# Performance work log

Hardware: AMD Instinct MI355X
Metric: run time of the kernel (lower is better)

The kernel has to match this reference:

```python
import jax, jax.numpy as jnp
import numpy as np

HIDDEN = 768
HEADS = 12
HEAD_DIM = HIDDEN // HEADS
BETA = 0.5
BANDWIDTH = 1.0
D_INTRINSIC = 3
LN_EPS = 1e-12


def setup_inputs() -> dict:
    key = jax.random.key(0)
    ks = jax.random.split(key, 10)
    B, S, E = 2, 2048, HIDDEN
    sc = 1.0 / np.sqrt(E)
    return {
        "hidden_states": jax.random.normal(ks[0], (B, S, E), jnp.float32),
        "attention_mask": jnp.zeros((B, S), jnp.float32),
        "Wq": jax.random.normal(ks[1], (E, E), jnp.float32) * sc,
        "bq": jax.random.normal(ks[2], (E,), jnp.float32) * 0.02,
        "Wv": jax.random.normal(ks[3], (E, E), jnp.float32) * sc,
        "bv": jax.random.normal(ks[4], (E,), jnp.float32) * 0.02,
        "Wo": jax.random.normal(ks[5], (E, E), jnp.float32) * sc,
        "bo": jax.random.normal(ks[6], (E,), jnp.float32) * 0.02,
        "ln_g": jnp.ones((E,), jnp.float32),
        "ln_b": jnp.zeros((E,), jnp.float32),
    }


def _layernorm(x, g, b, eps=LN_EPS):
    mu = jnp.mean(x, axis=-1, keepdims=True)
    var = jnp.mean((x - mu) ** 2, axis=-1, keepdims=True)
    return (x - mu) * jax.lax.rsqrt(var + eps) * g + b


def reference(hidden_states, attention_mask, Wq, bq, Wv, bv, Wo, bo, ln_g, ln_b):
    B, S, E = hidden_states.shape
    H, D = HEADS, HEAD_DIM
    # projections (torch Linear: x @ W.T + b)
    q = (hidden_states @ Wq.T + bq).reshape(B, S, H, D).transpose(0, 2, 1, 3)  # [B,H,S,D]
    v = (hidden_states @ Wv.T + bv).reshape(B, S, H, D).transpose(0, 2, 1, 3)  # [B,H,S,D]
    # pairwise Euclidean distance (cdist) via norm expansion, safe sqrt
    qn = jnp.sum(q * q, axis=-1)  # [B,H,S]
    d2 = qn[:, :, :, None] + qn[:, :, None, :] - 2.0 * jnp.einsum("bhid,bhjd->bhij", q, q)
    dist = jnp.sqrt(jnp.maximum(d2, 1e-12))  # [B,H,S,S]
    # mask: positions with attention_mask < 0 get distance 2
    keep = (attention_mask >= 0)  # [B,S]
    pair_keep = keep[:, None, :, None] & keep[:, None, None, :]  # [B,1,S,S]
    dist = jnp.where(pair_keep, dist, 2.0)
    # power-law score + softmax
    attn_score = (1.0 + dist / (BANDWIDTH ** 0.5)) ** (-D_INTRINSIC - BETA)
    attn = jax.nn.softmax(attn_score, axis=-1)
    out = jnp.einsum("bhij,bhjd->bhid", attn, v)  # [B,H,S,D]
    out = out.transpose(0, 2, 1, 3).reshape(B, S, E)
    # ModelSelfOutput: dense + residual + LayerNorm (dropout=0, eval)
    out = out @ Wo.T + bo
    return _layernorm(out + hidden_states, ln_g, ln_b)
```

## Files before the change

kernel.cpp:

```cpp
#include <hip/hip_runtime.h>
#include <hip/hip_bf16.h>
#include <cstdint>
#include <cstddef>

#define S_LEN 2048
#define NH 12
#define HD 64
#define EDIM 768

typedef short bf16x8 __attribute__((ext_vector_type(8)));
typedef float f32x4  __attribute__((ext_vector_type(4)));
typedef float f32x2  __attribute__((ext_vector_type(2)));

__device__ __forceinline__ unsigned short f2bf(float f) {
    return __bfloat16_as_ushort(__float2bfloat16(f));
}
__device__ __forceinline__ float bf2f(unsigned short u) {
    union { unsigned int i; float f; } x;
    x.i = ((unsigned int)u) << 16;
    return x.f;
}
__device__ __forceinline__ float rsq_f32(float x) {
#if __has_builtin(__builtin_amdgcn_rsqf)
    return __builtin_amdgcn_rsqf(x);
#else
    return __builtin_amdgcn_rcpf(__builtin_amdgcn_sqrtf(x));
#endif
}

__global__ __launch_bounds__(256) void precast_kernel(
    const float* __restrict__ hs, const float* __restrict__ Wq,
    const float* __restrict__ Wv, const float* __restrict__ Wo,
    unsigned short* __restrict__ hsb, unsigned short* __restrict__ Wqvb,
    unsigned short* __restrict__ Wob)
{
    const int i4 = blockIdx.x * 256 + threadIdx.x;
    const float* src;
    unsigned short* dst;
    int rel;
    if (i4 < 786432)        { src = hs; dst = hsb;            rel = i4; }
    else if (i4 < 933888)   { src = Wq; dst = Wqvb;           rel = i4 - 786432; }
    else if (i4 < 1081344)  { src = Wv; dst = Wqvb + 589824;  rel = i4 - 933888; }
    else                    { src = Wo; dst = Wob;            rel = i4 - 1081344; }
    float4 v = ((const float4*)src)[rel];
    ushort4 o;
    o.x = f2bf(v.x); o.y = f2bf(v.y); o.z = f2bf(v.z); o.w = f2bf(v.w);
    ((ushort4*)dst)[rel] = o;
}

__global__ __launch_bounds__(256) void qv_gemm(
    const unsigned short* __restrict__ hsb, const unsigned short* __restrict__ Wqvb,
    const float* __restrict__ bq, const float* __restrict__ bv,
    unsigned short* __restrict__ Qb, unsigned short* __restrict__ Vt,
    float* __restrict__ qn)
{
    __shared__ __align__(16) unsigned short As[64][40];
    __shared__ __align__(16) unsigned short Bs[128][40];

    const int t  = threadIdx.x;
    const int m0 = blockIdx.y << 6;
    const int c0 = blockIdx.x << 7;
    const bool isQ = (c0 < EDIM);
    const float* bias = isQ ? bq : bv;
    const int cb = isQ ? c0 : (c0 - EDIM);

    const int w  = t >> 6;
    const int l  = t & 63;
    const int ll = l & 15;
    const int lq = l >> 4;
    const int wx = w & 1;
    const int wy = w >> 1;

    const int srowA = t & 63;
    const int skA   = (t >> 6) << 3;
    const int srowB = t & 127;
    const int skB   = (t >> 7) << 4;

    f32x4 acc[2][4];
#pragma unroll
    for (int m = 0; m < 2; m++)
#pragma unroll
        for (int n = 0; n < 4; n++) acc[m][n] = (f32x4){0.f, 0.f, 0.f, 0.f};

    for (int k0 = 0; k0 < EDIM; k0 += 32) {
        bf16x8 va  = *(const bf16x8*)(hsb  + (size_t)(m0 + srowA) * EDIM + k0 + skA);
        bf16x8 vb0 = *(const bf16x8*)(Wqvb + (size_t)(c0 + srowB) * EDIM + k0 + skB);
        bf16x8 vb1 = *(const bf16x8*)(Wqvb + (size_t)(c0 + srowB) * EDIM + k0 + skB + 8);
        __syncthreads();
        *(bf16x8*)&As[srowA][skA]     = va;
        *(bf16x8*)&Bs[srowB][skB]     = vb0;
        *(bf16x8*)&Bs[srowB][skB + 8] = vb1;
        __syncthreads();
        bf16x8 aF[2], bF[4];
#pragma unroll
        for (int m = 0; m < 2; m++)
            aF[m] = *(const bf16x8*)&As[(wy << 5) + (m << 4) + ll][lq << 3];
#pragma unroll
        for (int n = 0; n < 4; n++)
            bF[n] = *(const bf16x8*)&Bs[(wx << 6) + (n << 4) + ll][lq << 3];
#pragma unroll
        for (int m = 0; m < 2; m++)
#pragma unroll
            for (int n = 0; n < 4; n++)
                acc[m][n] = __builtin_amdgcn_mfma_f32_16x16x32_bf16(aF[m], bF[n], acc[m][n], 0, 0, 0);
    }

    const int hcol0 = cb + (wx << 6);
    const int h = hcol0 >> 6;
    const int rowbase = m0 + (wy << 5);
    const int b = rowbase >> 11;
    const int sbase = rowbase & 2047;

    if (isQ) {
#pragma unroll
        for (int m = 0; m < 2; m++) {
#pragma unroll
            for (int r = 0; r < 4; r++) {
                const int si = sbase + (m << 4) + (lq << 2) + r;
                unsigned short* qrow = Qb + ((size_t)(b * NH + h) * S_LEN + si) * HD;
                float qsq = 0.f;
#pragma unroll
                for (int n = 0; n < 4; n++) {
                    unsigned short u = f2bf(acc[m][n][r] + bias[hcol0 + (n << 4) + ll]);
                    qrow[(n << 4) + ll] = u;
                    float f = bf2f(u);
                    qsq += f * f;
                }
                qsq += __shfl_xor(qsq, 1);
                qsq += __shfl_xor(qsq, 2);
                qsq += __shfl_xor(qsq, 4);
                qsq += __shfl_xor(qsq, 8);
                if (ll == 0) qn[(b * NH + h) * S_LEN + si] = qsq;
            }
        }
    } else {
#pragma unroll
        for (int m = 0; m < 2; m++) {
            const int si = sbase + (m << 4) + (lq << 2);
#pragma unroll
            for (int n = 0; n < 4; n++) {
                ushort4 o;
                o.x = f2bf(acc[m][n][0] + bias[hcol0 + (n << 4) + ll]);
                o.y = f2bf(acc[m][n][1] + bias[hcol0 + (n << 4) + ll]);
                o.z = f2bf(acc[m][n][2] + bias[hcol0 + (n << 4) + ll]);
                o.w = f2bf(acc[m][n][3] + bias[hcol0 + (n << 4) + ll]);
                *(ushort4*)&Vt[((size_t)(b * NH + h) * HD + (n << 4) + ll) * S_LEN + si] = o;
            }
        }
    }
}

template<int CUR>
__device__ __forceinline__ void attn_tile32(
    int j0, int jn,
    const unsigned short* __restrict__ Qbase,
    const unsigned short* __restrict__ Vbase,
    const float* __restrict__ qnb, const float* __restrict__ mb,
    int ll, int lq,
    const bf16x8 (&aQ)[2][2],
    const f32x2 (&qni2)[2][2], const f32x2 (&keepi2)[2][2],
    const bf16x8& ones,
    f32x4 (&oacc)[2][4], f32x4 (&wacc)[2],
    bf16x8 (&nb0)[2], bf16x8 (&nb1)[2],
    bf16x8 (&vbuf)[2][4],
    float (&qnjv)[2][2], float (&kjm)[2][2],
    unsigned short (&Wt)[2][2][16][40])
{
    constexpr int PRV = CUR ^ 1;
    __builtin_amdgcn_wave_barrier();
#pragma unroll
    for (int m = 0; m < 4; m++)
        vbuf[CUR][m] = *(const bf16x8*)(Vbase + (size_t)((m << 4) + ll) * S_LEN + j0 + (lq << 3));
    f32x4 s[2][2];
#pragma unroll
    for (int s2 = 0; s2 < 2; s2++)
#pragma unroll
        for (int n = 0; n < 2; n++) {
            f32x4 c = (f32x4){0.f, 0.f, 0.f, 0.f};
            c = __builtin_amdgcn_mfma_f32_16x16x32_bf16(aQ[s2][0], nb0[n], c, 0, 0, 0);
            c = __builtin_amdgcn_mfma_f32_16x16x32_bf16(aQ[s2][1], nb1[n], c, 0, 0, 0);
            s[s2][n] = c;
        }
#pragma unroll
    for (int n = 0; n < 2; n++) {
        const unsigned short* bp = Qbase + (size_t)(jn + (n << 4) + ll) * HD + (lq << 3);
        nb0[n] = *(const bf16x8*)bp;
        nb1[n] = *(const bf16x8*)(bp + 32);
        int jc = jn + (n << 4) + ll;
        qnjv[PRV][n] = qnb[jc];
        kjm[PRV][n]  = (mb[jc] >= 0.f) ? 1.f : 0.f;
    }
#pragma unroll
    for (int s2 = 0; s2 < 2; s2++) {
        bf16x8 aP = *(const bf16x8*)&Wt[PRV][s2][ll][lq << 3];
#pragma unroll
        for (int m = 0; m < 4; m++)
            oacc[s2][m] = __builtin_amdgcn_mfma_f32_16x16x32_bf16(aP, vbuf[PRV][m], oacc[s2][m], 0, 0, 0);
        wacc[s2] = __builtin_amdgcn_mfma_f32_16x16x32_bf16(aP, ones, wacc[s2], 0, 0, 0);
    }
#pragma unroll
    for (int s2 = 0; s2 < 2; s2++)
#pragma unroll
        for (int n = 0; n < 2; n++) {
            const f32x2 qv = (f32x2)(qnjv[CUR][n]);
            const f32x2 kj = (f32x2)(kjm[CUR][n]);
#pragma unroll
            for (int pr = 0; pr < 2; pr++) {
                f32x2 sp = { s[s2][n][2*pr], s[s2][n][2*pr + 1] };
                f32x2 d2 = __builtin_elementwise_fma(sp, (f32x2)(-2.f), qni2[s2][pr] + qv);
                d2 = __builtin_elementwise_max(d2, (f32x2)(1e-12f));
                f32x2 dist = { __builtin_amdgcn_sqrtf(d2.x), __builtin_amdgcn_sqrtf(d2.y) };
                f32x2 km = keepi2[s2][pr] * kj;
                f32x2 x  = __builtin_elementwise_fma(km, dist + (f32x2)(-2.f), (f32x2)(3.f));
                f32x2 x2 = x * x;
                f32x2 x4 = x2 * x2;
                f32x2 x6 = x4 * x2;
                f32x2 x7 = x6 * x;
                f32x2 p  = { rsq_f32(x7.x), rsq_f32(x7.y) };
                f32x2 wv = __builtin_elementwise_fma(
                    __builtin_elementwise_fma(
                        __builtin_elementwise_fma(
                            __builtin_elementwise_fma((f32x2)(0.041666668f), p, (f32x2)(0.16666667f)),
                            p, (f32x2)(0.5f)),
                        p, (f32x2)(1.0f)),
                    p, (f32x2)(1.0f));
                union { float f; unsigned int u; } c0, c1;
                c0.f = wv.x; c1.f = wv.y;
                Wt[CUR][s2][(lq << 2) + 2*pr    ][(n << 4) + ll] = (unsigned short)((c0.u + 0x8000u) >> 16);
                Wt[CUR][s2][(lq << 2) + 2*pr + 1][(n << 4) + ll] = (unsigned short)((c1.u + 0x8000u) >> 16);
            }
        }
}

__global__ __launch_bounds__(256) void attn_kernel(
    const unsigned short* __restrict__ Qb, const unsigned short* __restrict__ Vt,
    const float* __restrict__ qn, const float* __restrict__ mask,
    unsigned short* __restrict__ AObf)
{
    __shared__ __align__(16) unsigned short Wt[4][2][2][16][40];

    const int t  = threadIdx.x;
    const int w  = t >> 6;
    const int l  = t & 63;
    const int ll = l & 15;
    const int lq = l >> 4;
    const int id = blockIdx.x;
    const int ib = id / 24;
    const int bh = id - ib * 24;
    const int b  = bh / NH;
    const int h  = bh - b * NH;
    const int iw = ib << 5;

    const unsigned short* Qbase = Qb + ((size_t)bh << 17);
    const unsigned short* Vbase = Vt + ((size_t)bh << 17);
    const float* qnb = qn + (bh << 11);
    const float* mb  = mask + (b << 11);

    unsigned short (&Wtw)[2][2][16][40] = Wt[w];

    const int tbase = w << 4;
    const int jb    = tbase << 5;

    bf16x8 aQ[2][2];
#pragma unroll
    for (int s2 = 0; s2 < 2; s2++) {
        const unsigned short* qp = Qbase + (size_t)(iw + (s2 << 4) + ll) * HD + (lq << 3);
        aQ[s2][0] = *(const bf16x8*)qp;
        aQ[s2][1] = *(const bf16x8*)(qp + 32);
    }

    f32x2 qni2[2][2], keepi2[2][2];
#pragma unroll
    for (int s2 = 0; s2 < 2; s2++)
#pragma unroll
        for (int pr = 0; pr < 2; pr++) {
            int r0 = iw + (s2 << 4) + (lq << 2) + 2*pr;
            qni2[s2][pr]   = (f32x2){ qnb[r0], qnb[r0 + 1] };
            keepi2[s2][pr] = (f32x2){ (mb[r0] >= 0.f) ? 1.f : 0.f,
                                      (mb[r0 + 1] >= 0.f) ? 1.f : 0.f };
        }

    bf16x8 ones;
#pragma unroll
    for (int i = 0; i < 8; i++) ones[i] = (short)0x3F80;

    f32x4 oacc[2][4];
#pragma unroll
    for (int s2 = 0; s2 < 2; s2++)
#pragma unroll
        for (int m = 0; m < 4; m++) oacc[s2][m] = (f32x4){0.f, 0.f, 0.f, 0.f};
    f32x4 wacc[2];
    wacc[0] = (f32x4){0.f, 0.f, 0.f, 0.f};
    wacc[1] = (f32x4){0.f, 0.f, 0.f, 0.f};

    bf16x8 nb0[2], nb1[2];
    float qnjv[2][2], kjm[2][2];
#pragma unroll
    for (int n = 0; n < 2; n++) {
        const unsigned short* bp = Qbase + (size_t)(jb + (n << 4) + ll) * HD + (lq << 3);
        nb0[n] = *(const bf16x8*)bp;
        nb1[n] = *(const bf16x8*)(bp + 32);
        int jc = jb + (n << 4) + ll;
        qnjv[0][n] = qnb[jc];
        kjm[0][n]  = (mb[jc] >= 0.f) ? 1.f : 0.f;
    }
    bf16x8 vbuf[2][4];

    {
#pragma unroll
        for (int m = 0; m < 4; m++)
            vbuf[0][m] = *(const bf16x8*)(Vbase + (size_t)((m << 4) + ll) * S_LEN + jb + (lq << 3));
        f32x4 s[2][2];
#pragma unroll
        for (int s2 = 0; s2 < 2; s2++)
#pragma unroll
            for (int n = 0; n < 2; n++) {
                f32x4 c = (f32x4){0.f, 0.f, 0.f, 0.f};
                c = __builtin_amdgcn_mfma_f32_16x16x32_bf16(aQ[s2][0], nb0[n], c, 0, 0, 0);
                c = __builtin_amdgcn_mfma_f32_16x16x32_bf16(aQ[s2][1], nb1[n], c, 0, 0, 0);
                s[s2][n] = c;
            }
#pragma unroll
        for (int n = 0; n < 2; n++) {
            const unsigned short* bp = Qbase + (size_t)(jb + 32 + (n << 4) + ll) * HD + (lq << 3);
            nb0[n] = *(const bf16x8*)bp;
            nb1[n] = *(const bf16x8*)(bp + 32);
            int jc = jb + 32 + (n << 4) + ll;
            qnjv[1][n] = qnb[jc];
            kjm[1][n]  = (mb[jc] >= 0.f) ? 1.f : 0.f;
        }
#pragma unroll
        for (int s2 = 0; s2 < 2; s2++)
#pragma unroll
            for (int n = 0; n < 2; n++) {
                const f32x2 qv = (f32x2)(qnjv[0][n]);
                const f32x2 kj = (f32x2)(kjm[0][n]);
#pragma unroll
                for (int pr = 0; pr < 2; pr++) {
                    f32x2 sp = { s[s2][n][2*pr], s[s2][n][2*pr + 1] };
                    f32x2 d2 = __builtin_elementwise_fma(sp, (f32x2)(-2.f), qni2[s2][pr] + qv);
                    d2 = __builtin_elementwise_max(d2, (f32x2)(1e-12f));
                    f32x2 dist = { __builtin_amdgcn_sqrtf(d2.x), __builtin_amdgcn_sqrtf(d2.y) };
                    f32x2 km = keepi2[s2][pr] * kj;
                    f32x2 x  = __builtin_elementwise_fma(km, dist + (f32x2)(-2.f), (f32x2)(3.f));
                    f32x2 x2 = x * x;
                    f32x2 x4 = x2 * x2;
                    f32x2 x6 = x4 * x2;
                    f32x2 x7 = x6 * x;
                    f32x2 p  = { rsq_f32(x7.x), rsq_f32(x7.y) };
                    f32x2 wv = __builtin_elementwise_fma(
                        __builtin_elementwise_fma(
                            __builtin_elementwise_fma(
                                __builtin_elementwise_fma((f32x2)(0.041666668f), p, (f32x2)(0.16666667f)),
                                p, (f32x2)(0.5f)),
                            p, (f32x2)(1.0f)),
                        p, (f32x2)(1.0f));
                    union { float f; unsigned int u; } c0, c1;
                    c0.f = wv.x; c1.f = wv.y;
                    Wtw[0][s2][(lq << 2) + 2*pr    ][(n << 4) + ll] = (unsigned short)((c0.u + 0x8000u) >> 16);
                    Wtw[0][s2][(lq << 2) + 2*pr + 1][(n << 4) + ll] = (unsigned short)((c1.u + 0x8000u) >> 16);
                }
            }
    }

    for (int tt = tbase + 1; tt <= tbase + 13; tt += 2) {
        attn_tile32<1>(tt << 5, (tt + 1) << 5, Qbase, Vbase, qnb, mb, ll, lq,
                       aQ, qni2, keepi2, ones, oacc, wacc, nb0, nb1, vbuf, qnjv, kjm, Wtw);
        attn_tile32<0>((tt + 1) << 5, (tt + 2) << 5, Qbase, Vbase, qnb, mb, ll, lq,
                       aQ, qni2, keepi2, ones, oacc, wacc, nb0, nb1, vbuf, qnjv, kjm, Wtw);
    }
    attn_tile32<1>((tbase + 15) << 5, 0, Qbase, Vbase, qnb, mb, ll, lq,
                   aQ, qni2, keepi2, ones, oacc, wacc, nb0, nb1, vbuf, qnjv, kjm, Wtw);

    __builtin_amdgcn_wave_barrier();
#pragma unroll
    for (int s2 = 0; s2 < 2; s2++) {
        bf16x8 aP = *(const bf16x8*)&Wtw[1][s2][ll][lq << 3];
#pragma unroll
        for (int m = 0; m < 4; m++)
            oacc[s2][m] = __builtin_amdgcn_mfma_f32_16x16x32_bf16(aP, vbuf[1][m], oacc[s2][m], 0, 0, 0);
        wacc[s2] = __builtin_amdgcn_mfma_f32_16x16x32_bf16(aP, ones, wacc[s2], 0, 0, 0);
    }

    float* red = (float*)Wt;
    __syncthreads();
    if (w >= 2) {
        float* p = red + (((w - 2) << 6) + l);
#pragma unroll
        for (int s2 = 0; s2 < 2; s2++)
#pragma unroll
            for (int m = 0; m < 4; m++)
#pragma unroll
                for (int r = 0; r < 4; r++)
                    p[((((s2 << 2) + m) << 2) + r) * 128] = oacc[s2][m][r];
#pragma unroll
        for (int s2 = 0; s2 < 2; s2++)
#pragma unroll
            for (int r = 0; r < 4; r++)
                p[(32 + (s2 << 2) + r) * 128] = wacc[s2][r];
    }
    __syncthreads();
    if (w < 2) {
        float* p = red + ((w << 6) + l);
#pragma unroll
        for (int s2 = 0; s2 < 2; s2++)
#pragma unroll
            for (int m = 0; m < 4; m++)
#pragma unroll
                for (int r = 0; r < 4; r++)
                    oacc[s2][m][r] += p[((((s2 << 2) + m) << 2) + r) * 128];
#pragma unroll
        for (int s2 = 0; s2 < 2; s2++)
#pragma unroll
            for (int r = 0; r < 4; r++)
                wacc[s2][r] += p[(32 + (s2 << 2) + r) * 128];
    }
    __syncthreads();
    if (w == 1) {
        float* p = red + l;
#pragma unroll
        for (int s2 = 0; s2 < 2; s2++)
#pragma unroll
            for (int m = 0; m < 4; m++)
#pragma unroll
                for (int r = 0; r < 4; r++)
                    p[((((s2 << 2) + m) << 2) + r) * 128] = oacc[s2][m][r];
#pragma unroll
        for (int s2 = 0; s2 < 2; s2++)
#pragma unroll
            for (int r = 0; r < 4; r++)
                p[(32 + (s2 << 2) + r) * 128] = wacc[s2][r];
    }
    __syncthreads();
    if (w == 0) {
        float* p = red + l;
#pragma unroll
        for (int s2 = 0; s2 < 2; s2++)
#pragma unroll
            for (int m = 0; m < 4; m++)
#pragma unroll
                for (int r = 0; r < 4; r++)
                    oacc[s2][m][r] += p[((((s2 << 2) + m) << 2) + r) * 128];
#pragma unroll
        for (int s2 = 0; s2 < 2; s2++)
#pragma unroll
            for (int r = 0; r < 4; r++)
                wacc[s2][r] += p[(32 + (s2 << 2) + r) * 128];

#pragma unroll
        for (int s2 = 0; s2 < 2; s2++)
#pragma unroll
            for (int r = 0; r < 4; r++) {
                float inv = 1.0f / wacc[s2][r];
                const int row = iw + (s2 << 4) + (lq << 2) + r;
                unsigned short* dst = AObf + (size_t)((b << 11) + row) * EDIM + (h << 6);
#pragma unroll
                for (int m = 0; m < 4; m++)
                    dst[(m << 4) + ll] = f2bf(oacc[s2][m][r] * inv);
            }
    }
}

__global__ __launch_bounds__(256) void oproj_gemm(
    const unsigned short* __restrict__ AObf, const unsigned short* __restrict__ Wob,
    const float* __restrict__ bo, const float* __restrict__ hs,
    float* __restrict__ TMP)
{
    __shared__ __align__(16) unsigned short As[64][40];
    __shared__ __align__(16) unsigned short Bs[64][40];

    const int t  = threadIdx.x;
    const int m0 = blockIdx.y << 6;
    const int c0 = blockIdx.x << 6;

    const int w  = t >> 6;
    const int l  = t & 63;
    const int ll = l & 15;
    const int lq = l >> 4;
    const int wx = w & 1;
    const int wy = w >> 1;

    const int srow = t & 63;
    const int sk   = (t >> 6) << 3;

    f32x4 acc[2][2];
#pragma unroll
    for (int m = 0; m < 2; m++)
#pragma unroll
        for (int n = 0; n < 2; n++) acc[m][n] = (f32x4){0.f, 0.f, 0.f, 0.f};

    for (int k0 = 0; k0 < EDIM; k0 += 32) {
        bf16x8 va = *(const bf16x8*)(AObf + (size_t)(m0 + srow) * EDIM + k0 + sk);
        bf16x8 vb = *(const bf16x8*)(Wob  + (size_t)(c0 + srow) * EDIM + k0 + sk);
        __syncthreads();
        *(bf16x8*)&As[srow][sk] = va;
        *(bf16x8*)&Bs[srow][sk] = vb;
        __syncthreads();
        bf16x8 aF[2], bF[2];
#pragma unroll
        for (int m = 0; m < 2; m++)
            aF[m] = *(const bf16x8*)&As[(wy << 5) + (m << 4) + ll][lq << 3];
#pragma unroll
        for (int n = 0; n < 2; n++)
            bF[n] = *(const bf16x8*)&Bs[(wx << 5) + (n << 4) + ll][lq << 3];
#pragma unroll
        for (int m = 0; m < 2; m++)
#pragma unroll
            for (int n = 0; n < 2; n++)
                acc[m][n] = __builtin_amdgcn_mfma_f32_16x16x32_bf16(aF[m], bF[n], acc[m][n], 0, 0, 0);
    }

#pragma unroll
    for (int m = 0; m < 2; m++) {
#pragma unroll
        for (int r = 0; r < 4; r++) {
            const int row = m0 + (wy << 5) + (m << 4) + (lq << 2) + r;
#pragma unroll
            for (int n = 0; n < 2; n++) {
                const int col = c0 + (wx << 5) + (n << 4) + ll;
                TMP[(size_t)row * EDIM + col] =
                    acc[m][n][r] + bo[col] + hs[(size_t)row * EDIM + col];
            }
        }
    }
}

__global__ __launch_bounds__(256) void ln_kernel(
    const float* __restrict__ X, const float* __restrict__ g,
    const float* __restrict__ be, float* __restrict__ out)
{
    const int row = blockIdx.x;
    const int t = threadIdx.x;
    const float* x = X + (size_t)row * EDIM;

    float s = 0.f, sq = 0.f;
#pragma unroll
    for (int c = t; c < EDIM; c += 256) {
        float v = x[c];
        s += v; sq += v * v;
    }
#pragma unroll
    for (int m = 1; m < 64; m <<= 1) {
        s  += __shfl_xor(s, m);
        sq += __shfl_xor(sq, m);
    }
    __shared__ float ss[4], ssq[4];
    const int w = t >> 6;
    if ((t & 63) == 0) { ss[w] = s; ssq[w] = sq; }
    __syncthreads();
    s  = ss[0] + ss[1] + ss[2] + ss[3];
    sq = ssq[0] + ssq[1] + ssq[2] + ssq[3];
    const float mu  = s * (1.f / EDIM);
    const float var = sq * (1.f / EDIM) - mu * mu;
    const float rstd = 1.0f / sqrtf(var + 1e-12f);

#pragma unroll
    for (int c = t; c < EDIM; c += 256) {
        out[(size_t)row * EDIM + c] = (x[c] - mu) * rstd * g[c] + be[c];
    }
}

extern "C" void kernel_launch(void* const* d_in, const int* in_sizes, int n_in,
                              void* d_out, int out_size, void* d_ws, size_t ws_size,
                              hipStream_t stream) {
    const float* hs   = (const float*)d_in[0];
    const float* mask = (const float*)d_in[1];
    const float* Wq   = (const float*)d_in[2];
    const float* bq   = (const float*)d_in[3];
    const float* Wv   = (const float*)d_in[4];
    const float* bv   = (const float*)d_in[5];
    const float* Wo   = (const float*)d_in[6];
    const float* bo   = (const float*)d_in[7];
    const float* g    = (const float*)d_in[8];
    const float* be   = (const float*)d_in[9];

    char* w8 = (char*)d_ws;
    unsigned short* Qb   = (unsigned short*)(w8);
    unsigned short* Vt   = (unsigned short*)(w8 +  6291456);
    float*          qn   = (float*)        (w8 + 12582912);
    unsigned short* AObf = (unsigned short*)(w8 + 12779520);
    unsigned short* hsb  = (unsigned short*)(w8 + 19070976);
    unsigned short* Wqvb = (unsigned short*)(w8 + 25362432);
    unsigned short* Wob  = (unsigned short*)(w8 + 27721728);
    float*          TMP  = (float*)(w8);

    precast_kernel<<<dim3(4800),    256, 0, stream>>>(hs, Wq, Wv, Wo, hsb, Wqvb, Wob);
    qv_gemm       <<<dim3(12, 64),  256, 0, stream>>>(hsb, Wqvb, bq, bv, Qb, Vt, qn);
    attn_kernel   <<<dim3(1536),    256, 0, stream>>>(Qb, Vt, qn, mask, AObf);
    oproj_gemm    <<<dim3(12, 64),  256, 0, stream>>>(AObf, Wob, bo, hs, TMP);
    ln_kernel     <<<dim3(4096),    256, 0, stream>>>(TMP, g, be, (float*)d_out);
}
```

Baseline: 250.5 us.

## Double-buffer projection GEMMs with direct global-to-LDS loads and XOR swizzle

Rewrites the K-loop of the QV and output-projection GEMMs so tiles are copied straight from global memory into LDS through global_load_lds, double-buffered so the next tile's load overlaps the current tile's MFMAs. The padded LDS rows are replaced by unpadded rows with an XOR swizzle to avoid bank conflicts, and each iteration needs one barrier instead of two. This removes the register staging and some synchronisation. It risks correctness if the async LDS writes are not waited on before the barrier, and these GEMMs are probably a small share of total time next to the attention kernel.

Result: faster. 232.0 us (median of 3 runs) (-7.4%).

```diff
diff --git a/kernel.cpp b/kernel.cpp
--- a/kernel.cpp
+++ b/kernel.cpp
@@ -26,6 +26,15 @@
 #else
     return __builtin_amdgcn_rcpf(__builtin_amdgcn_sqrtf(x));
 #endif
+}
+
+__device__ __forceinline__ int swz4(int r) { return (r + (r >> 2)) & 3; }
+
+__device__ __forceinline__ void gload16(const unsigned short* g, unsigned short* l) {
+    __builtin_amdgcn_global_load_lds(
+        (const __attribute__((address_space(1))) unsigned int*)g,
+        (__attribute__((address_space(3))) unsigned int*)l,
+        16, 0, 0);
 }
 
 __global__ __launch_bounds__(256) void precast_kernel(
@@ -54,8 +63,8 @@
     unsigned short* __restrict__ Qb, unsigned short* __restrict__ Vt,
     float* __restrict__ qn)
 {
-    __shared__ __align__(16) unsigned short As[64][40];
-    __shared__ __align__(16) unsigned short Bs[128][40];
+    __shared__ __align__(16) unsigned short As[2][64][32];
+    __shared__ __align__(16) unsigned short Bs[2][128][32];
 
     const int t  = threadIdx.x;
     const int m0 = blockIdx.y << 6;
@@ -71,10 +80,12 @@
     const int wx = w & 1;
     const int wy = w >> 1;
 
-    const int srowA = t & 63;
-    const int skA   = (t >> 6) << 3;
-    const int srowB = t & 127;
-    const int skB   = (t >> 7) << 4;
+    const int arow  = (w << 4) + (l >> 2);
+    const int brow0 = (w << 5) + (l >> 2);
+    const int brow1 = brow0 + 16;
+    const unsigned short* aSrc  = hsb  + (size_t)(m0 + arow ) * EDIM + (((l & 3) ^ swz4(arow )) << 3);
+    const unsigned short* bSrc0 = Wqvb + (size_t)(c0 + brow0) * EDIM + (((l & 3) ^ swz4(brow0)) << 3);
+    const unsigned short* bSrc1 = Wqvb + (size_t)(c0 + brow1) * EDIM + (((l & 3) ^ swz4(brow1)) << 3);
 
     f32x4 acc[2][4];
 #pragma unroll
@@ -82,27 +93,36 @@
 #pragma unroll
         for (int n = 0; n < 4; n++) acc[m][n] = (f32x4){0.f, 0.f, 0.f, 0.f};
 
+    gload16(aSrc,  &As[0][w << 4][0]);
+    gload16(bSrc0, &Bs[0][w << 5][0]);
+    gload16(bSrc1, &Bs[0][(w << 5) + 16][0]);
+    __syncthreads();
+
+    int cur = 0;
     for (int k0 = 0; k0 < EDIM; k0 += 32) {
-        bf16x8 va  = *(const bf16x8*)(hsb  + (size_t)(m0 + srowA) * EDIM + k0 + skA);
-        bf16x8 vb0 = *(const bf16x8*)(Wqvb + (size_t)(c0 + srowB) * EDIM + k0 + skB);
-        bf16x8 vb1 = *(const bf16x8*)(Wqvb + (size_t)(c0 + srowB) * EDIM + k0 + skB + 8);
-        __syncthreads();
-        *(bf16x8*)&As[srowA][skA]     = va;
-        *(bf16x8*)&Bs[srowB][skB]     = vb0;
-        *(bf16x8*)&Bs[srowB][skB + 8] = vb1;
-        __syncthreads();
+        if (k0 + 32 < EDIM) {
+            gload16(aSrc  + k0 + 32, &As[cur ^ 1][w << 4][0]);
+            gload16(bSrc0 + k0 + 32, &Bs[cur ^ 1][w << 5][0]);
+            gload16(bSrc1 + k0 + 32, &Bs[cur ^ 1][(w << 5) + 16][0]);
+        }
         bf16x8 aF[2], bF[4];
 #pragma unroll
-        for (int m = 0; m < 2; m++)
-            aF[m] = *(const bf16x8*)&As[(wy << 5) + (m << 4) + ll][lq << 3];
-#pragma unroll
-        for (int n = 0; n < 4; n++)
-            bF[n] = *(const bf16x8*)&Bs[(wx << 6) + (n << 4) + ll][lq << 3];
+        for (int m = 0; m < 2; m++) {
+            const int row = (wy << 5) + (m << 4) + ll;
+            aF[m] = *(const bf16x8*)&As[cur][row][(lq ^ swz4(row)) << 3];
+        }
+#pragma unroll
+        for (int n = 0; n < 4; n++) {
+            const int row = (wx << 6) + (n << 4) + ll;
+            bF[n] = *(const bf16x8*)&Bs[cur][row][(lq ^ swz4(row)) << 3];
+        }
 #pragma unroll
         for (int m = 0; m < 2; m++)
 #pragma unroll
             for (int n = 0; n < 4; n++)
                 acc[m][n] = __builtin_amdgcn_mfma_f32_16x16x32_bf16(aF[m], bF[n], acc[m][n], 0, 0, 0);
+        __syncthreads();
+        cur ^= 1;
     }
 
     const int hcol0 = cb + (wx << 6);
@@ -466,8 +486,8 @@
     const float* __restrict__ bo, const float* __restrict__ hs,
     float* __restrict__ TMP)
 {
-    __shared__ __align__(16) unsigned short As[64][40];
-    __shared__ __align__(16) unsigned short Bs[64][40];
+    __shared__ __align__(16) unsigned short As[2][64][32];
+    __shared__ __align__(16) unsigned short Bs[2][64][32];
 
     const int t  = threadIdx.x;
     const int m0 = blockIdx.y << 6;
@@ -480,8 +500,9 @@
     const int wx = w & 1;
     const int wy = w >> 1;
 
-    const int srow = t & 63;
-    const int sk   = (t >> 6) << 3;
+    const int srow = (w << 4) + (l >> 2);
+    const unsigned short* aSrc = AObf + (size_t)(m0 + srow) * EDIM + (((l & 3) ^ swz4(srow)) << 3);
+    const unsigned short* bSrc = Wob  + (size_t)(c0 + srow) * EDIM + (((l & 3) ^ swz4(srow)) << 3);
 
     f32x4 acc[2][2];
 #pragma unroll
@@ -489,25 +510,34 @@
 #pragma unroll
         for (int n = 0; n < 2; n++) acc[m][n] = (f32x4){0.f, 0.f, 0.f, 0.f};
 
+    gload16(aSrc, &As[0][w << 4][0]);
+    gload16(bSrc, &Bs[0][w << 4][0]);
+    __syncthreads();
+
+    int cur = 0;
     for (int k0 = 0; k0 < EDIM; k0 += 32) {
-        bf16x8 va = *(const bf16x8*)(AObf + (size_t)(m0 + srow) * EDIM + k0 + sk);
-        bf16x8 vb = *(const bf16x8*)(Wob  + (size_t)(c0 + srow) * EDIM + k0 + sk);
-        __syncthreads();
-        *(bf16x8*)&As[srow][sk] = va;
-        *(bf16x8*)&Bs[srow][sk] = vb;
-        __syncthreads();
+        if (k0 + 32 < EDIM) {
+            gload16(aSrc + k0 + 32, &As[cur ^ 1][w << 4][0]);
+            gload16(bSrc + k0 + 32, &Bs[cur ^ 1][w << 4][0]);
+        }
         bf16x8 aF[2], bF[2];
 #pragma unroll
-        for (int m = 0; m < 2; m++)
-            aF[m] = *(const bf16x8*)&As[(wy << 5) + (m << 4) + ll][lq << 3];
-#pragma unroll
-        for (int n = 0; n < 2; n++)
-            bF[n] = *(const bf16x8*)&Bs[(wx << 5) + (n << 4) + ll][lq << 3];
+        for (int m = 0; m < 2; m++) {
+            const int row = (wy << 5) + (m << 4) + ll;
+            aF[m] = *(const bf16x8*)&As[cur][row][(lq ^ swz4(row)) << 3];
+        }
+#pragma unroll
+        for (int n = 0; n < 2; n++) {
+            const int row = (wx << 5) + (n << 4) + ll;
+            bF[n] = *(const bf16x8*)&Bs[cur][row][(lq ^ swz4(row)) << 3];
+        }
 #pragma unroll
         for (int m = 0; m < 2; m++)
 #pragma unroll
             for (int n = 0; n < 2; n++)
                 acc[m][n] = __builtin_amdgcn_mfma_f32_16x16x32_bf16(aF[m], bF[n], acc[m][n], 0, 0, 0);
+        __syncthreads();
+        cur ^= 1;
     }
 
 #pragma unroll
```
